# Kernel tuning notes

Measured on AMD Instinct MI355X. Metric: run time of the kernel, lower is better.

## Reference

```python
import jax, jax.numpy as jnp
import numpy as np

N = 100000
E = 6400000
IN_CH = 128
HID = 5
H1 = 2
OUT = 10
H2 = 1
EPS_BN = 1e-5


def glorot(key, shape):
    fan = shape[0] + shape[-1]
    s = jnp.sqrt(6.0 / fan)
    return jax.random.uniform(key, shape, jnp.float32, -s, s)


def setup_inputs() -> dict:
    key = jax.random.key(0)
    ks = jax.random.split(key, 12)
    x = jax.random.normal(ks[0], (N, IN_CH), jnp.float32)
    edge_index = jax.random.randint(ks[1], (2, E), 0, N, jnp.int64)
    return {
        "x": x,
        "W1": glorot(ks[2], (IN_CH, H1 * HID)),
        "a_src1": glorot(ks[3], (H1, HID)),
        "a_dst1": glorot(ks[4], (H1, HID)),
        "b1": jnp.zeros((H1 * HID,), jnp.float32),
        "gamma1": jnp.ones((H1 * HID,), jnp.float32),
        "beta1": jnp.zeros((H1 * HID,), jnp.float32),
        "W2": glorot(ks[5], (H1 * HID, H2 * OUT)),
        "a_src2": glorot(ks[6], (H2, OUT)),
        "a_dst2": glorot(ks[7], (H2, OUT)),
        "b2": jnp.zeros((OUT,), jnp.float32),
        "edge_index": edge_index,
    }


def gat_conv(x, src, dst, W, a_src, a_dst, bias, heads, out_ch, concat):
    n = x.shape[0]
    h = (x @ W).reshape(n, heads, out_ch)          # [N,H,C]
    alpha_s = (h * a_src).sum(-1)                  # [N,H]
    alpha_d = (h * a_dst).sum(-1)                  # [N,H]
    e = jax.nn.leaky_relu(alpha_s[src] + alpha_d[dst], 0.2)  # [E,H]
    emax = jax.ops.segment_max(e, dst, num_segments=n)
    emax = jnp.where(jnp.isfinite(emax), emax, 0.0)
    ex = jnp.exp(e - jax.lax.stop_gradient(emax)[dst])
    denom = jax.ops.segment_sum(ex, dst, num_segments=n)
    alpha = ex / (denom[dst] + 1e-16)              # edge softmax by target
    msg = h[src] * alpha[..., None]                # [E,H,C]
    out = jax.ops.segment_sum(msg, dst, num_segments=n)
    out = out.reshape(n, heads * out_ch) if concat else out.mean(axis=1)
    return out + bias


def batch_norm(x, gamma, beta):
    mu = x.mean(0)
    var = ((x - mu) ** 2).mean(0)
    return (x - mu) * jax.lax.rsqrt(var + EPS_BN) * gamma + beta


def reference(x, W1, a_src1, a_dst1, b1, gamma1, beta1, W2, a_src2, a_dst2, b2, edge_index):
    n = x.shape[0]
    loop = jnp.arange(n, dtype=edge_index.dtype)   # add_self_loops=True
    src = jnp.concatenate([edge_index[0], loop])
    dst = jnp.concatenate([edge_index[1], loop])
    h = gat_conv(x, src, dst, W1, a_src1, a_dst1, b1, H1, HID, True)
    h = batch_norm(h, gamma1, beta1)
    h = jax.nn.elu(h)
    out = gat_conv(h, src, dst, W2, a_src2, a_dst2, b2, H2, OUT, False)
    return out
```

## Files before the change

kernel.cpp:

```cpp
#include <hip/hip_runtime.h>
#include <hip/hip_fp16.h>
#include <math.h>

#define NN 100000
#define NE 6400000
#define INCH 128
#define BSH 7
#define BW (1 << BSH)
#define NBKT ((NN + BW - 1) / BW)
#define NBP 784
#define BCAP 9216
#define BIN_CH 8192
#define BNP 800

__device__ inline float pkh(float a, float b) {
  __half2 h = __floats2half2_rn(a, b);
  return __uint_as_float(*reinterpret_cast<unsigned int*>(&h));
}
__device__ inline float2 uph(float f) {
  unsigned int b = __float_as_uint(f);
  __half2 h = *reinterpret_cast<__half2*>(&b);
  return __half22float2(h);
}

__global__ __launch_bounds__(256) void k_count(const int* __restrict__ ei,
                                               int* __restrict__ cntmat) {
  __shared__ int cnt4[4][NBKT];
  int t = threadIdx.x;
  int w = t >> 6;
  for (int i = t; i < 4 * NBKT; i += 256) (&cnt4[0][0])[i] = 0;
  __syncthreads();
  int c0 = blockIdx.x * BIN_CH;
  int c1 = c0 + BIN_CH < NE ? c0 + BIN_CH : NE;
  for (int i = c0 + t; i < c1; i += 256)
    atomicAdd(&cnt4[w][ei[NE + i] >> BSH], 1);
  __syncthreads();
  for (int b = t; b < NBKT; b += 256)
    cntmat[(size_t)b * NBP + blockIdx.x] =
        cnt4[0][b] + cnt4[1][b] + cnt4[2][b] + cnt4[3][b];
}

__global__ __launch_bounds__(64) void k_scanb(const int* __restrict__ cntmat,
                                              int* __restrict__ basemat,
                                              int* __restrict__ bcnt) {
  int j = blockIdx.x;
  int lane = threadIdx.x;
  int carry = 0;
  for (int i0 = 0; i0 < NBKT; i0 += 64) {
    int i = i0 + lane;
    int v0 = (i < NBKT) ? cntmat[(size_t)j * NBP + i] : 0;
    int v = v0;
#pragma unroll
    for (int off = 1; off < 64; off <<= 1) {
      int u = __shfl_up(v, off, 64);
      if (lane >= off) v += u;
    }
    if (i < NBKT) basemat[(size_t)i * NBP + j] = carry + v - v0;
    carry += __shfl(v, 63, 64);
  }
  if (lane == 0) bcnt[j] = carry;
}

__global__ __launch_bounds__(256) void k_scatter2(
    const int* __restrict__ ei, const int* __restrict__ cntmat,
    const int* __restrict__ basemat, unsigned int* __restrict__ pairs) {
  __shared__ int offs[NBKT];
  __shared__ int cur[NBKT];
  __shared__ int gbase[NBKT];
  __shared__ int scanp[256];
  __shared__ unsigned int stage[BIN_CH];
  __shared__ unsigned short sbkt[BIN_CH];
  int t = threadIdx.x;
  int chunk = blockIdx.x;
  int myb0 = t * 4;
  int tots[4];
  int asum = 0;
#pragma unroll
  for (int j = 0; j < 4; j++) {
    int b = myb0 + j;
    int tt = (b < NBKT) ? cntmat[(size_t)b * NBP + chunk] : 0;
    tots[j] = tt;
    asum += tt;
  }
  for (int b = t; b < NBKT; b += 256)
    gbase[b] = basemat[(size_t)chunk * NBP + b];
  scanp[t] = asum;
  __syncthreads();
  for (int off = 1; off < 256; off <<= 1) {
    int v = (t >= off) ? scanp[t - off] : 0;
    __syncthreads();
    scanp[t] += v;
    __syncthreads();
  }
  int run = (t == 0) ? 0 : scanp[t - 1];
#pragma unroll
  for (int j = 0; j < 4; j++) {
    int b = myb0 + j;
    if (b < NBKT) {
      offs[b] = run;
      cur[b] = run;
      run += tots[j];
    }
  }
  __syncthreads();
  int c0 = chunk * BIN_CH;
  int c1 = c0 + BIN_CH < NE ? c0 + BIN_CH : NE;
  for (int i = c0 + t; i < c1; i += 256) {
    int s = ei[i], d = ei[NE + i];
    int bkt = d >> BSH;
    int pos = atomicAdd(&cur[bkt], 1);
    stage[pos] = ((unsigned int)s << BSH) | (unsigned int)(d & (BW - 1));
    sbkt[pos] = (unsigned short)bkt;
  }
  __syncthreads();
  int total = c1 - c0;
  for (int i = t; i < total; i += 256) {
    unsigned int e = stage[i];
    int b = sbkt[i];
    int gp = gbase[b] + (i - offs[b]);
    if (gp < BCAP) pairs[(size_t)b * BCAP + gp] = e;
  }
}

__global__ __launch_bounds__(512, 6) void k_sortb(
    const int* __restrict__ bcnt, unsigned int* __restrict__ pairs,
    unsigned int* __restrict__ oc) {
  __shared__ int cnt8[8][BW];
  __shared__ int wb[8][BW];
  __shared__ int tot[BW];
  __shared__ int scanbuf[BW];
  __shared__ unsigned int sorted[BCAP];
  int t = threadIdx.x;
  int w = t >> 6;
  int b = blockIdx.x;
  int base_n = b << BSH;
  for (int i = t; i < 8 * BW; i += 512) (&cnt8[0][0])[i] = 0;
  __syncthreads();
  int cntb = bcnt[b];
  cntb = cntb > BCAP ? BCAP : cntb;
  unsigned int* pp = pairs + (size_t)b * BCAP;
  for (int k = t; k < cntb; k += 512)
    atomicAdd(&cnt8[w][pp[k] & (BW - 1)], 1);
  __syncthreads();
  if (t < BW) {
    int tt = 0;
#pragma unroll
    for (int j = 0; j < 8; j++) tt += cnt8[j][t];
    tot[t] = tt;
    scanbuf[t] = tt;
  }
  __syncthreads();
  for (int step = 1; step < BW; step <<= 1) {
    int v = 0;
    if (t < BW && t >= step) v = scanbuf[t - step];
    __syncthreads();
    if (t < BW) scanbuf[t] += v;
    __syncthreads();
  }
  if (t < BW) {
    int run = scanbuf[t] - tot[t];
    int n = base_n + t;
    if (n < NN) oc[n] = ((unsigned int)run << 16) | (unsigned int)tot[t];
#pragma unroll
    for (int j = 0; j < 8; j++) { wb[j][t] = run; run += cnt8[j][t]; cnt8[j][t] = 0; }
  }
  __syncthreads();
  for (int k = t; k < cntb; k += 512) {
    unsigned int e = pp[k];
    int dl = e & (BW - 1);
    int pos = wb[w][dl] + atomicAdd(&cnt8[w][dl], 1);
    sorted[pos] = e >> BSH;
  }
  __syncthreads();
  for (int k = t; k < cntb; k += 512) pp[k] = sorted[k];
}

__global__ __launch_bounds__(256) void k_l1_node(
    const float* __restrict__ x, const float* __restrict__ W1,
    const float* __restrict__ a_src1, const float* __restrict__ a_dst1,
    float* __restrict__ h1, float2* __restrict__ ad1) {
  __shared__ float Wt[10 * INCH];
  __shared__ float asw[10], adw[10];
  for (int i = threadIdx.x; i < 10 * INCH; i += blockDim.x) {
    int c = i / 10, k = i - c * 10;
    Wt[k * INCH + c] = W1[i];
  }
  if (threadIdx.x < 10) {
    asw[threadIdx.x] = a_src1[threadIdx.x];
    adw[threadIdx.x] = a_dst1[threadIdx.x];
  }
  __syncthreads();
  int n = blockIdx.x * blockDim.x + threadIdx.x;
  if (n >= NN) return;
  const float4* xr = (const float4*)(x + (size_t)n * INCH);
  const float4* Wt4 = (const float4*)Wt;
  float acc[10];
#pragma unroll
  for (int k = 0; k < 10; k++) acc[k] = 0.f;
#pragma unroll 8
  for (int c4 = 0; c4 < INCH / 4; c4++) {
    float4 xv = xr[c4];
#pragma unroll
    for (int k = 0; k < 10; k++) {
      float4 wv = Wt4[k * (INCH / 4) + c4];
      acc[k] += xv.x * wv.x + xv.y * wv.y + xv.z * wv.z + xv.w * wv.w;
    }
  }
  float s0 = 0.f, s1 = 0.f, d0 = 0.f, d1 = 0.f;
#pragma unroll
  for (int j = 0; j < 5; j++) {
    s0 += acc[j] * asw[j];
    s1 += acc[5 + j] * asw[5 + j];
    d0 += acc[j] * adw[j];
    d1 += acc[5 + j] * adw[5 + j];
  }
  float4* hrow = (float4*)(h1 + (size_t)n * 8);
  hrow[0] = make_float4(pkh(acc[0], acc[1]), pkh(acc[2], acc[3]),
                        pkh(acc[4], acc[5]), pkh(acc[6], acc[7]));
  hrow[1] = make_float4(pkh(acc[8], acc[9]), 0.f, s0, s1);
  ad1[n] = make_float2(d0, d1);
}

__global__ __launch_bounds__(512, 8) void k_l1_aggs(
    const unsigned int* __restrict__ sorted_g, const unsigned int* __restrict__ oc,
    const float* __restrict__ h1, const float2* __restrict__ ad1,
    const float* __restrict__ b1, float* __restrict__ g1,
    float* __restrict__ bn_part) {
  __shared__ __align__(16) unsigned int sorted[BCAP];
  __shared__ float biasS[10];
  __shared__ float bn_lds[8 * 20];
  int t = threadIdx.x;
  int w = t >> 6;
  int b = blockIdx.x;
  int base_n = b << BSH;
  if (t < 10) biasS[t] = b1[t];
  {
    const uint4* pp4 = (const uint4*)(sorted_g + (size_t)b * BCAP);
    uint4* s4 = (uint4*)sorted;
    for (int k = t; k < BCAP / 4; k += 512) s4[k] = pp4[k];
  }
  __syncthreads();
  int node = t >> 2;
  int part = t & 3;
  int n = base_n + node;
  bool valid = n < NN;
  unsigned int ocv = valid ? oc[n] : 0u;
  int s0i = (int)(ocv >> 16);
  int c = (int)(ocv & 0xffffu);
  float2 adn = valid ? ad1[n] : make_float2(0.f, 0.f);
  float acc[10];
#pragma unroll
  for (int j = 0; j < 10; j++) acc[j] = 0.f;
  float den0 = 0.f, den1 = 0.f;
  for (int k = part; k < c; k += 4) {
    int s = (int)sorted[s0i + k];
    const float4* hs = (const float4*)(h1 + (size_t)s * 8);
    float4 ra = hs[0], rb = hs[1];
    float e0 = rb.z + adn.x; e0 = e0 > 0.f ? e0 : 0.2f * e0;
    float e1 = rb.w + adn.y; e1 = e1 > 0.f ? e1 : 0.2f * e1;
    float x0 = expf(e0), x1 = expf(e1);
    float2 h01 = uph(ra.x), h23 = uph(ra.y), h45 = uph(ra.z), h67 = uph(ra.w),
           h89 = uph(rb.x);
    acc[0] += x0 * h01.x;  acc[1] += x0 * h01.y;  acc[2] += x0 * h23.x;
    acc[3] += x0 * h23.y;  acc[4] += x0 * h45.x;
    acc[5] += x1 * h45.y;  acc[6] += x1 * h67.x;  acc[7] += x1 * h67.y;
    acc[8] += x1 * h89.x;  acc[9] += x1 * h89.y;
    den0 += x0; den1 += x1;
  }
#pragma unroll
  for (int j = 0; j < 10; j++) {
    acc[j] += __shfl_xor(acc[j], 1, 64);
    acc[j] += __shfl_xor(acc[j], 2, 64);
  }
  den0 += __shfl_xor(den0, 1, 64); den0 += __shfl_xor(den0, 2, 64);
  den1 += __shfl_xor(den1, 1, 64); den1 += __shfl_xor(den1, 2, 64);
  float v[10];
#pragma unroll
  for (int j = 0; j < 10; j++) v[j] = 0.f;
  if (part == 0 && valid) {
    const float4* hs = (const float4*)(h1 + (size_t)n * 8);
    float4 ra = hs[0], rb = hs[1];
    float e0 = rb.z + adn.x; e0 = e0 > 0.f ? e0 : 0.2f * e0;
    float e1 = rb.w + adn.y; e1 = e1 > 0.f ? e1 : 0.2f * e1;
    float x0 = expf(e0), x1 = expf(e1);
    float2 h01 = uph(ra.x), h23 = uph(ra.y), h45 = uph(ra.z), h67 = uph(ra.w),
           h89 = uph(rb.x);
    acc[0] += x0 * h01.x;  acc[1] += x0 * h01.y;  acc[2] += x0 * h23.x;
    acc[3] += x0 * h23.y;  acc[4] += x0 * h45.x;
    acc[5] += x1 * h45.y;  acc[6] += x1 * h67.x;  acc[7] += x1 * h67.y;
    acc[8] += x1 * h89.x;  acc[9] += x1 * h89.y;
    den0 += x0; den1 += x1;
    float i0 = 1.f / (den0 + 1e-16f), i1 = 1.f / (den1 + 1e-16f);
#pragma unroll
    for (int j = 0; j < 5; j++) v[j] = acc[j] * i0 + biasS[j];
#pragma unroll
    for (int j = 5; j < 10; j++) v[j] = acc[j] * i1 + biasS[j];
    float4* gr = (float4*)(g1 + (size_t)n * 12);
    gr[0] = make_float4(v[0], v[1], v[2], v[3]);
    gr[1] = make_float4(v[4], v[5], v[6], v[7]);
    gr[2] = make_float4(v[8], v[9], 0.f, 0.f);
  }
  float s[20];
#pragma unroll
  for (int j = 0; j < 10; j++) { s[j] = v[j]; s[10 + j] = v[j] * v[j]; }
#pragma unroll
  for (int j = 0; j < 20; j++) {
    s[j] += __shfl_down(s[j], 4, 64);
    s[j] += __shfl_down(s[j], 8, 64);
    s[j] += __shfl_down(s[j], 16, 64);
    s[j] += __shfl_down(s[j], 32, 64);
  }
  if ((t & 63) == 0) {
#pragma unroll
    for (int j = 0; j < 20; j++) bn_lds[w * 20 + j] = s[j];
  }
  __syncthreads();
  if (t == 0) {
#pragma unroll
    for (int j = 0; j < 20; j++) {
      float acc20 = 0.f;
#pragma unroll
      for (int ww = 0; ww < 8; ww++) acc20 += bn_lds[ww * 20 + j];
      bn_part[j * BNP + b] = acc20;
    }
  }
}

__global__ __launch_bounds__(64) void k_bnred(const float* __restrict__ bn_part,
                                              float* __restrict__ bns) {
  int j = blockIdx.x;
  int lane = threadIdx.x;
  float s = 0.f;
  for (int b = lane; b < NBKT; b += 64) s += bn_part[j * BNP + b];
#pragma unroll
  for (int off = 32; off > 0; off >>= 1) s += __shfl_down(s, off, 64);
  if (lane == 0) bns[j] = s;
}

__global__ __launch_bounds__(256) void k_l2_node(
    const float* __restrict__ g1, const float* __restrict__ bns,
    const float* __restrict__ gamma1, const float* __restrict__ beta1,
    const float* __restrict__ W2, const float* __restrict__ a_src2,
    const float* __restrict__ a_dst2, float* __restrict__ h2,
    float* __restrict__ ad2) {
  __shared__ float scale[10], shift[10], W2s[100], a2s[10], a2d[10];
  if (threadIdx.x < 10) {
    int j = threadIdx.x;
    float mu = bns[j] * (1.f / NN);
    float var = bns[10 + j] * (1.f / NN) - mu * mu;
    float rs = rsqrtf(var + 1e-5f);
    scale[j] = rs * gamma1[j];
    shift[j] = beta1[j] - mu * rs * gamma1[j];
    a2s[j] = a_src2[j];
    a2d[j] = a_dst2[j];
  }
  for (int i = threadIdx.x; i < 100; i += blockDim.x) W2s[i] = W2[i];
  __syncthreads();
  int n = blockIdx.x * blockDim.x + threadIdx.x;
  if (n >= NN) return;
  const float4* gr = (const float4*)(g1 + (size_t)n * 12);
  float4 g0 = gr[0], g1v = gr[1], g2 = gr[2];
  float hv[10] = {g0.x, g0.y, g0.z, g0.w, g1v.x, g1v.y, g1v.z, g1v.w, g2.x, g2.y};
#pragma unroll
  for (int j = 0; j < 10; j++) {
    float t = hv[j] * scale[j] + shift[j];
    hv[j] = t > 0.f ? t : expm1f(t);
  }
  float o[10];
#pragma unroll
  for (int k = 0; k < 10; k++) o[k] = 0.f;
#pragma unroll
  for (int c = 0; c < 10; c++) {
#pragma unroll
    for (int k = 0; k < 10; k++) o[k] += hv[c] * W2s[c * 10 + k];
  }
  float ss = 0.f, sd = 0.f;
#pragma unroll
  for (int k = 0; k < 10; k++) { ss += o[k] * a2s[k]; sd += o[k] * a2d[k]; }
  float4* hr = (float4*)(h2 + (size_t)n * 8);
  hr[0] = make_float4(pkh(o[0], o[1]), pkh(o[2], o[3]), pkh(o[4], o[5]),
                      pkh(o[6], o[7]));
  hr[1] = make_float4(pkh(o[8], o[9]), 0.f, ss, 0.f);
  ad2[n] = sd;
}

__global__ __launch_bounds__(512, 8) void k_l2_aggs(
    const unsigned int* __restrict__ sorted_g, const unsigned int* __restrict__ oc,
    const float* __restrict__ h2, const float* __restrict__ ad2,
    const float* __restrict__ b2, float* __restrict__ out) {
  __shared__ __align__(16) unsigned int sorted[BCAP];
  __shared__ float biasS[10];
  int t = threadIdx.x;
  int b = blockIdx.x;
  int base_n = b << BSH;
  if (t < 10) biasS[t] = b2[t];
  {
    const uint4* pp4 = (const uint4*)(sorted_g + (size_t)b * BCAP);
    uint4* s4 = (uint4*)sorted;
    for (int k = t; k < BCAP / 4; k += 512) s4[k] = pp4[k];
  }
  __syncthreads();
  int node = t >> 2;
  int part = t & 3;
  int n = base_n + node;
  bool valid = n < NN;
  unsigned int ocv = valid ? oc[n] : 0u;
  int s0i = (int)(ocv >> 16);
  int c = (int)(ocv & 0xffffu);
  float adn = valid ? ad2[n] : 0.f;
  float acc[10];
#pragma unroll
  for (int j = 0; j < 10; j++) acc[j] = 0.f;
  float den = 0.f;
  for (int k = part; k < c; k += 4) {
    int s = (int)sorted[s0i + k];
    const float4* hs = (const float4*)(h2 + (size_t)s * 8);
    float4 ra = hs[0], rb = hs[1];
    float ee = rb.z + adn; ee = ee > 0.f ? ee : 0.2f * ee;
    float xv = expf(ee);
    float2 h01 = uph(ra.x), h23 = uph(ra.y), h45 = uph(ra.z), h67 = uph(ra.w),
           h89 = uph(rb.x);
    acc[0] += xv * h01.x;  acc[1] += xv * h01.y;  acc[2] += xv * h23.x;
    acc[3] += xv * h23.y;  acc[4] += xv * h45.x;  acc[5] += xv * h45.y;
    acc[6] += xv * h67.x;  acc[7] += xv * h67.y;  acc[8] += xv * h89.x;
    acc[9] += xv * h89.y;
    den += xv;
  }
#pragma unroll
  for (int j = 0; j < 10; j++) {
    acc[j] += __shfl_xor(acc[j], 1, 64);
    acc[j] += __shfl_xor(acc[j], 2, 64);
  }
  den += __shfl_xor(den, 1, 64); den += __shfl_xor(den, 2, 64);
  if (part == 0 && valid) {
    const float4* hs = (const float4*)(h2 + (size_t)n * 8);
    float4 ra = hs[0], rb = hs[1];
    float ee = rb.z + adn; ee = ee > 0.f ? ee : 0.2f * ee;
    float xv = expf(ee);
    float2 h01 = uph(ra.x), h23 = uph(ra.y), h45 = uph(ra.z), h67 = uph(ra.w),
           h89 = uph(rb.x);
    acc[0] += xv * h01.x;  acc[1] += xv * h01.y;  acc[2] += xv * h23.x;
    acc[3] += xv * h23.y;  acc[4] += xv * h45.x;  acc[5] += xv * h45.y;
    acc[6] += xv * h67.x;  acc[7] += xv * h67.y;  acc[8] += xv * h89.x;
    acc[9] += xv * h89.y;
    den += xv;
    float inv = 1.f / (den + 1e-16f);
    float2* orow = (float2*)(out + (size_t)n * 10);
    orow[0] = make_float2(acc[0] * inv + biasS[0], acc[1] * inv + biasS[1]);
    orow[1] = make_float2(acc[2] * inv + biasS[2], acc[3] * inv + biasS[3]);
    orow[2] = make_float2(acc[4] * inv + biasS[4], acc[5] * inv + biasS[5]);
    orow[3] = make_float2(acc[6] * inv + biasS[6], acc[7] * inv + biasS[7]);
    orow[4] = make_float2(acc[8] * inv + biasS[8], acc[9] * inv + biasS[9]);
  }
}

extern "C" void kernel_launch(void* const* d_in, const int* in_sizes, int n_in,
                              void* d_out, int out_size, void* d_ws, size_t ws_size,
                              hipStream_t stream) {
  const float* x      = (const float*)d_in[0];
  const float* W1     = (const float*)d_in[1];
  const float* a_src1 = (const float*)d_in[2];
  const float* a_dst1 = (const float*)d_in[3];
  const float* b1     = (const float*)d_in[4];
  const float* gamma1 = (const float*)d_in[5];
  const float* beta1  = (const float*)d_in[6];
  const float* W2     = (const float*)d_in[7];
  const float* a_src2 = (const float*)d_in[8];
  const float* a_dst2 = (const float*)d_in[9];
  const float* b2     = (const float*)d_in[10];
  const int*   ei     = (const int*)d_in[11];
  float* out = (float*)d_out;

  int* bcnt = (int*)d_ws;
  unsigned int* pairs = (unsigned int*)d_ws + 1024;
  float* h1 = (float*)(pairs + (size_t)NBKT * BCAP);
  float* ad1 = h1 + (size_t)NN * 8;
  float* g1 = ad1 + (size_t)NN * 2;
  float* h2 = g1 + (size_t)NN * 12;
  float* ad2 = h2 + (size_t)NN * 8;
  float* bn_part = ad2 + NN;
  float* bns = bn_part + 20 * BNP;
  int* cntmat = (int*)(bns + 20 + 12);
  int* basemat = cntmat + (size_t)NBKT * NBP;
  unsigned int* oc = (unsigned int*)(basemat + (size_t)NBKT * NBP);

  const int B = 256;
  const int gN = (NN + B - 1) / B;
  const int gBin = (NE + BIN_CH - 1) / BIN_CH;

  k_count<<<gBin, B, 0, stream>>>(ei, cntmat);
  k_scanb<<<NBKT, 64, 0, stream>>>(cntmat, basemat, bcnt);
  k_scatter2<<<gBin, B, 0, stream>>>(ei, cntmat, basemat, pairs);
  k_sortb<<<NBKT, 512, 0, stream>>>(bcnt, pairs, oc);
  k_l1_node<<<gN, B, 0, stream>>>(x, W1, a_src1, a_dst1, h1, (float2*)ad1);
  k_l1_aggs<<<NBKT, 512, 0, stream>>>(pairs, oc, h1, (const float2*)ad1, b1,
                                      g1, bn_part);
  k_bnred<<<20, 64, 0, stream>>>(bn_part, bns);
  k_l2_node<<<gN, B, 0, stream>>>(g1, bns, gamma1, beta1, W2, a_src2, a_dst2,
                                  h2, ad2);
  k_l2_aggs<<<NBKT, 512, 0, stream>>>(pairs, oc, h2, ad2, b2, out);
}
```

Before: 353.3 us.

## Replace two-level bucket sort with direct per-node atomic counting sort

Replaces the chunked bucket count, scan, staged scatter and in-bucket sort pipeline with a per-node global atomic histogram, a per-bucket scan, and a direct scatter through per-node atomic cursors. This removes two passes and the LDS-heavy bucket sort, at the cost of heavy global atomics on 100k counters and uncoalesced scatter writes. The aggregation kernels now copy only the used part of each bucket into LDS rather than the full capacity. Edge order within a node becomes nondeterministic, which can change float summation order.

New measurement: 1.041 ms. +194.7%, slower.

```diff
diff --git a/kernel.cpp b/kernel.cpp
--- a/kernel.cpp
+++ b/kernel.cpp
@@ -8,9 +8,7 @@
 #define BSH 7
 #define BW (1 << BSH)
 #define NBKT ((NN + BW - 1) / BW)
-#define NBP 784
 #define BCAP 9216
-#define BIN_CH 8192
 #define BNP 800
 
 __device__ inline float pkh(float a, float b) {
@@ -23,156 +21,52 @@
   return __half22float2(h);
 }
 
-__global__ __launch_bounds__(256) void k_count(const int* __restrict__ ei,
-                                               int* __restrict__ cntmat) {
-  __shared__ int cnt4[4][NBKT];
-  int t = threadIdx.x;
-  int w = t >> 6;
-  for (int i = t; i < 4 * NBKT; i += 256) (&cnt4[0][0])[i] = 0;
-  __syncthreads();
-  int c0 = blockIdx.x * BIN_CH;
-  int c1 = c0 + BIN_CH < NE ? c0 + BIN_CH : NE;
-  for (int i = c0 + t; i < c1; i += 256)
-    atomicAdd(&cnt4[w][ei[NE + i] >> BSH], 1);
-  __syncthreads();
-  for (int b = t; b < NBKT; b += 256)
-    cntmat[(size_t)b * NBP + blockIdx.x] =
-        cnt4[0][b] + cnt4[1][b] + cnt4[2][b] + cnt4[3][b];
-}
-
-__global__ __launch_bounds__(64) void k_scanb(const int* __restrict__ cntmat,
-                                              int* __restrict__ basemat,
-                                              int* __restrict__ bcnt) {
-  int j = blockIdx.x;
-  int lane = threadIdx.x;
-  int carry = 0;
-  for (int i0 = 0; i0 < NBKT; i0 += 64) {
-    int i = i0 + lane;
-    int v0 = (i < NBKT) ? cntmat[(size_t)j * NBP + i] : 0;
-    int v = v0;
-#pragma unroll
-    for (int off = 1; off < 64; off <<= 1) {
-      int u = __shfl_up(v, off, 64);
-      if (lane >= off) v += u;
-    }
-    if (i < NBKT) basemat[(size_t)i * NBP + j] = carry + v - v0;
-    carry += __shfl(v, 63, 64);
-  }
-  if (lane == 0) bcnt[j] = carry;
-}
-
-__global__ __launch_bounds__(256) void k_scatter2(
-    const int* __restrict__ ei, const int* __restrict__ cntmat,
-    const int* __restrict__ basemat, unsigned int* __restrict__ pairs) {
-  __shared__ int offs[NBKT];
-  __shared__ int cur[NBKT];
-  __shared__ int gbase[NBKT];
-  __shared__ int scanp[256];
-  __shared__ unsigned int stage[BIN_CH];
-  __shared__ unsigned short sbkt[BIN_CH];
-  int t = threadIdx.x;
-  int chunk = blockIdx.x;
-  int myb0 = t * 4;
-  int tots[4];
-  int asum = 0;
-#pragma unroll
-  for (int j = 0; j < 4; j++) {
-    int b = myb0 + j;
-    int tt = (b < NBKT) ? cntmat[(size_t)b * NBP + chunk] : 0;
-    tots[j] = tt;
-    asum += tt;
-  }
-  for (int b = t; b < NBKT; b += 256)
-    gbase[b] = basemat[(size_t)chunk * NBP + b];
-  scanp[t] = asum;
-  __syncthreads();
-  for (int off = 1; off < 256; off <<= 1) {
-    int v = (t >= off) ? scanp[t - off] : 0;
-    __syncthreads();
-    scanp[t] += v;
-    __syncthreads();
-  }
-  int run = (t == 0) ? 0 : scanp[t - 1];
-#pragma unroll
-  for (int j = 0; j < 4; j++) {
-    int b = myb0 + j;
-    if (b < NBKT) {
-      offs[b] = run;
-      cur[b] = run;
-      run += tots[j];
-    }
-  }
-  __syncthreads();
-  int c0 = chunk * BIN_CH;
-  int c1 = c0 + BIN_CH < NE ? c0 + BIN_CH : NE;
-  for (int i = c0 + t; i < c1; i += 256) {
-    int s = ei[i], d = ei[NE + i];
-    int bkt = d >> BSH;
-    int pos = atomicAdd(&cur[bkt], 1);
-    stage[pos] = ((unsigned int)s << BSH) | (unsigned int)(d & (BW - 1));
-    sbkt[pos] = (unsigned short)bkt;
-  }
-  __syncthreads();
-  int total = c1 - c0;
-  for (int i = t; i < total; i += 256) {
-    unsigned int e = stage[i];
-    int b = sbkt[i];
-    int gp = gbase[b] + (i - offs[b]);
-    if (gp < BCAP) pairs[(size_t)b * BCAP + gp] = e;
-  }
-}
-
-__global__ __launch_bounds__(512, 6) void k_sortb(
-    const int* __restrict__ bcnt, unsigned int* __restrict__ pairs,
-    unsigned int* __restrict__ oc) {
-  __shared__ int cnt8[8][BW];
-  __shared__ int wb[8][BW];
-  __shared__ int tot[BW];
-  __shared__ int scanbuf[BW];
-  __shared__ unsigned int sorted[BCAP];
-  int t = threadIdx.x;
-  int w = t >> 6;
-  int b = blockIdx.x;
-  int base_n = b << BSH;
-  for (int i = t; i < 8 * BW; i += 512) (&cnt8[0][0])[i] = 0;
-  __syncthreads();
-  int cntb = bcnt[b];
-  cntb = cntb > BCAP ? BCAP : cntb;
-  unsigned int* pp = pairs + (size_t)b * BCAP;
-  for (int k = t; k < cntb; k += 512)
-    atomicAdd(&cnt8[w][pp[k] & (BW - 1)], 1);
-  __syncthreads();
-  if (t < BW) {
-    int tt = 0;
-#pragma unroll
-    for (int j = 0; j < 8; j++) tt += cnt8[j][t];
-    tot[t] = tt;
-    scanbuf[t] = tt;
-  }
-  __syncthreads();
-  for (int step = 1; step < BW; step <<= 1) {
-    int v = 0;
-    if (t < BW && t >= step) v = scanbuf[t - step];
-    __syncthreads();
-    if (t < BW) scanbuf[t] += v;
-    __syncthreads();
-  }
-  if (t < BW) {
-    int run = scanbuf[t] - tot[t];
-    int n = base_n + t;
-    if (n < NN) oc[n] = ((unsigned int)run << 16) | (unsigned int)tot[t];
-#pragma unroll
-    for (int j = 0; j < 8; j++) { wb[j][t] = run; run += cnt8[j][t]; cnt8[j][t] = 0; }
-  }
-  __syncthreads();
-  for (int k = t; k < cntb; k += 512) {
-    unsigned int e = pp[k];
-    int dl = e & (BW - 1);
-    int pos = wb[w][dl] + atomicAdd(&cnt8[w][dl], 1);
-    sorted[pos] = e >> BSH;
-  }
-  __syncthreads();
-  for (int k = t; k < cntb; k += 512) pp[k] = sorted[k];
+__global__ __launch_bounds__(256) void k_zero(int* __restrict__ nodecnt) {
+  int i = blockIdx.x * blockDim.x + threadIdx.x;
+  if (i < NN) nodecnt[i] = 0;
+}
+
+__global__ __launch_bounds__(256) void k_hist(const int* __restrict__ ei,
+                                              int* __restrict__ nodecnt) {
+  int i = blockIdx.x * blockDim.x + threadIdx.x;
+  if (i < NE) atomicAdd(&nodecnt[ei[NE + i]], 1);
+}
+
+__global__ __launch_bounds__(128) void k_nodescan(
+    const int* __restrict__ nodecnt, unsigned int* __restrict__ oc,
+    int* __restrict__ cursor, int* __restrict__ bcnt) {
+  __shared__ int wsum[2];
+  int b = blockIdx.x, t = threadIdx.x;
+  int lane = t & 63, w = t >> 6;
+  int n = (b << BSH) + t;
+  int c = (n < NN) ? nodecnt[n] : 0;
+  int v = c;
+#pragma unroll
+  for (int off = 1; off < 64; off <<= 1) {
+    int u = __shfl_up(v, off, 64);
+    if (lane >= off) v += u;
+  }
+  if (lane == 63) wsum[w] = v;
+  __syncthreads();
+  int base = (w == 1) ? wsum[0] : 0;
+  int start = base + v - c;
+  if (n < NN) {
+    oc[n] = ((unsigned int)start << 16) | (unsigned int)c;
+    cursor[n] = b * BCAP + start;
+  }
+  if (t == 127) bcnt[b] = wsum[0] + v;
+}
+
+__global__ __launch_bounds__(256) void k_sdir(const int* __restrict__ ei,
+                                              int* __restrict__ cursor,
+                                              unsigned int* __restrict__ pairs) {
+  int i = blockIdx.x * blockDim.x + threadIdx.x;
+  if (i >= NE) return;
+  int s = ei[i], d = ei[NE + i];
+  int pos = atomicAdd(&cursor[d], 1);
+  int b = d >> BSH;
+  unsigned int rel = (unsigned int)(pos - b * BCAP);
+  if (rel < BCAP) pairs[(size_t)b * BCAP + rel] = (unsigned int)s;
 }
 
 __global__ __launch_bounds__(256) void k_l1_node(
@@ -222,6 +116,7 @@
 }
 
 __global__ __launch_bounds__(512, 8) void k_l1_aggs(
+    const int* __restrict__ bcnt,
     const unsigned int* __restrict__ sorted_g, const unsigned int* __restrict__ oc,
     const float* __restrict__ h1, const float2* __restrict__ ad1,
     const float* __restrict__ b1, float* __restrict__ g1,
@@ -235,9 +130,12 @@
   int base_n = b << BSH;
   if (t < 10) biasS[t] = b1[t];
   {
+    int cb = bcnt[b];
+    cb = cb > BCAP ? BCAP : cb;
+    int n4 = (cb + 3) >> 2;
     const uint4* pp4 = (const uint4*)(sorted_g + (size_t)b * BCAP);
     uint4* s4 = (uint4*)sorted;
-    for (int k = t; k < BCAP / 4; k += 512) s4[k] = pp4[k];
+    for (int k = t; k < n4; k += 512) s4[k] = pp4[k];
   }
   __syncthreads();
   int node = t >> 2;
@@ -385,6 +283,7 @@
 }
 
 __global__ __launch_bounds__(512, 8) void k_l2_aggs(
+    const int* __restrict__ bcnt,
     const unsigned int* __restrict__ sorted_g, const unsigned int* __restrict__ oc,
     const float* __restrict__ h2, const float* __restrict__ ad2,
     const float* __restrict__ b2, float* __restrict__ out) {
@@ -395,9 +294,12 @@
   int base_n = b << BSH;
   if (t < 10) biasS[t] = b2[t];
   {
+    int cb = bcnt[b];
+    cb = cb > BCAP ? BCAP : cb;
+    int n4 = (cb + 3) >> 2;
     const uint4* pp4 = (const uint4*)(sorted_g + (size_t)b * BCAP);
     uint4* s4 = (uint4*)sorted;
-    for (int k = t; k < BCAP / 4; k += 512) s4[k] = pp4[k];
+    for (int k = t; k < n4; k += 512) s4[k] = pp4[k];
   }
   __syncthreads();
   int node = t >> 2;
@@ -480,23 +382,23 @@
   float* ad2 = h2 + (size_t)NN * 8;
   float* bn_part = ad2 + NN;
   float* bns = bn_part + 20 * BNP;
-  int* cntmat = (int*)(bns + 20 + 12);
-  int* basemat = cntmat + (size_t)NBKT * NBP;
-  unsigned int* oc = (unsigned int*)(basemat + (size_t)NBKT * NBP);
+  int* nodecnt = (int*)(bns + 20 + 12);
+  int* cursor = nodecnt + NN;
+  unsigned int* oc = (unsigned int*)(cursor + NN);
 
   const int B = 256;
   const int gN = (NN + B - 1) / B;
-  const int gBin = (NE + BIN_CH - 1) / BIN_CH;
-
-  k_count<<<gBin, B, 0, stream>>>(ei, cntmat);
-  k_scanb<<<NBKT, 64, 0, stream>>>(cntmat, basemat, bcnt);
-  k_scatter2<<<gBin, B, 0, stream>>>(ei, cntmat, basemat, pairs);
-  k_sortb<<<NBKT, 512, 0, stream>>>(bcnt, pairs, oc);
+  const int gE = (NE + B - 1) / B;
+
+  k_zero<<<gN, B, 0, stream>>>(nodecnt);
+  k_hist<<<gE, B, 0, stream>>>(ei, nodecnt);
+  k_nodescan<<<NBKT, 128, 0, stream>>>(nodecnt, oc, cursor, bcnt);
+  k_sdir<<<gE, B, 0, stream>>>(ei, cursor, pairs);
   k_l1_node<<<gN, B, 0, stream>>>(x, W1, a_src1, a_dst1, h1, (float2*)ad1);
-  k_l1_aggs<<<NBKT, 512, 0, stream>>>(pairs, oc, h1, (const float2*)ad1, b1,
-                                      g1, bn_part);
+  k_l1_aggs<<<NBKT, 512, 0, stream>>>(bcnt, pairs, oc, h1, (const float2*)ad1,
+                                      b1, g1, bn_part);
   k_bnred<<<20, 64, 0, stream>>>(bn_part, bns);
   k_l2_node<<<gN, B, 0, stream>>>(g1, bns, gamma1, beta1, W2, a_src2, a_dst2,
                                   h2, ad2);
-  k_l2_aggs<<<NBKT, 512, 0, stream>>>(pairs, oc, h2, ad2, b2, out);
-}
+  k_l2_aggs<<<NBKT, 512, 0, stream>>>(bcnt, pairs, oc, h2, ad2, b2, out);
+}
```
